# Kernel tuning notes

Measured on AMD Instinct MI355X. Metric: run time of the kernel, lower is better.

## Reference

```python
import jax, jax.numpy as jnp
import numpy as np

NUM_NODES = 1_200_000
NUM_FILLER = 200_000
NUM_PHYS = NUM_NODES - NUM_FILLER  # 1,000,000 physical nodes
NUM_MOVABLE = 900_000
NBX = NBY = 512
XL, XH, YL, YH = 0.0, 1000.0, 0.0, 1000.0
BSX = (XH - XL) / NBX
BSY = (YH - YL) / NBY
PIN_STRETCH = 1.4142135623730951
UNIT_PIN_CAP = 0.05
MAX_RATE = 1.5
MIN_RATE = 1.0 / MAX_RATE
K = 5  # max bins overlapped per dimension (span<=4.0, bin~1.95)


def _overlap_terms(lo, hi, bin_size, origin, nb):
    # lo, hi: [n] interval per node. Returns bin indices [n,K] and overlap lengths [n,K].
    il = jnp.clip(jnp.floor((lo - origin) / bin_size).astype(jnp.int32), 0, nb - 1)
    idx = il[:, None] + jnp.arange(K, dtype=jnp.int32)[None, :]
    valid = idx < nb
    idx = jnp.clip(idx, 0, nb - 1)
    b_lo = origin + idx.astype(lo.dtype) * bin_size
    ov = jnp.maximum(jnp.minimum(hi[:, None], b_lo + bin_size) - jnp.maximum(lo[:, None], b_lo), 0.0)
    return idx, jnp.where(valid, ov, 0.0)


def _forward(pos, node_size_x, node_size_y, flat_node2pin_start_map):
    P = NUM_PHYS
    sx, sy = node_size_x[:P], node_size_y[:P]
    # stretched half sizes: at least half a stretched bin
    hx = 0.5 * jnp.maximum(BSX * PIN_STRETCH, sx)
    hy = 0.5 * jnp.maximum(BSY * PIN_STRETCH, sy)
    cx = pos[:P] + 0.5 * sx
    cy = pos[NUM_NODES:NUM_NODES + P] + 0.5 * sy
    pw = (flat_node2pin_start_map[1:P + 1] - flat_node2pin_start_map[:P]).astype(pos.dtype)
    density = pw / (4.0 * hx * hy)  # pins per unit area over stretched bbox

    # stage 1: scatter stretched-bbox pin density into bin map
    ix, ovx = _overlap_terms(cx - hx, cx + hx, BSX, XL, NBX)  # [P,K]
    iy, ovy = _overlap_terms(cy - hy, cy + hy, BSY, YL, NBY)  # [P,K]
    contrib = ovx[:, :, None] * ovy[:, None, :] * density[:, None, None]  # [P,K,K]
    flat_idx = (ix[:, :, None] * NBY + iy[:, None, :]).reshape(-1)
    pin_map = jnp.zeros(NBX * NBY, dtype=pos.dtype).at[flat_idx].add(contrib.reshape(-1))

    # stage 2: pin utilization per bin, clamped adjust rate
    util = jnp.clip(pin_map / (BSX * BSY * UNIT_PIN_CAP), MIN_RATE, MAX_RATE)

    # stage 3: per movable node, integrate utilization over its (unstretched) bbox
    M = NUM_MOVABLE
    x_lo = pos[:M]
    x_hi = x_lo + node_size_x[:M]
    y_lo = pos[NUM_NODES:NUM_NODES + M]
    y_hi = y_lo + node_size_y[:M]
    jx, wx = _overlap_terms(x_lo, x_hi, BSX, XL, NBX)  # [M,K]
    jy, wy = _overlap_terms(y_lo, y_hi, BSY, YL, NBY)  # [M,K]
    u = util[jx[:, :, None] * NBY + jy[:, None, :]]  # [M,K,K]
    instance_pin_area = jnp.sum(wx[:, :, None] * wy[:, None, :] * u, axis=(1, 2))
    return instance_pin_area


def setup_inputs() -> dict:
    key = jax.random.key(0)
    k1, k2, k3, k4 = jax.random.split(key, 4)
    node_size_x = jax.random.uniform(k1, (NUM_NODES,), jnp.float32, 1.0, 4.0)
    node_size_y = jnp.full((NUM_NODES,), 2.0, jnp.float32)  # row height
    px = jax.random.uniform(k2, (NUM_NODES,), jnp.float32, 0.0, 995.0)
    py = jax.random.uniform(k3, (NUM_NODES,), jnp.float32, 0.0, 995.0)
    pos = jnp.concatenate([px, py])
    pin_counts = jax.random.randint(k4, (NUM_PHYS,), 1, 9, jnp.int32)
    flat = jnp.concatenate([jnp.zeros(1, jnp.int32), jnp.cumsum(pin_counts).astype(jnp.int32)])
    return {"pos": pos, "node_size_x": node_size_x, "node_size_y": node_size_y,
            "flat_node2pin_start_map": flat}


def reference(pos, node_size_x, node_size_y, flat_node2pin_start_map):
    return _forward(pos, node_size_x, node_size_y, flat_node2pin_start_map)
```

## Files before the change

kernel.cpp:

```cpp
#include <hip/hip_runtime.h>

#define NUM_NODES   1200000
#define NUM_FILLER  200000
#define NUM_PHYS    (NUM_NODES - NUM_FILLER)
#define NUM_MOVABLE 900000
#define NBX 512
#define NBY 512
#define NBINS (NBX * NBY)
#define BSX 1.953125f
#define BSY 1.953125f
#define PIN_STRETCH 1.4142135623730951f
#define CAP 0.19073486328125f
#define INV_CAP (1.0f / 0.19073486328125f)
#define MAX_RATE 1.5f
#define MIN_RATE (1.0f/1.5f)
#define K 5

#define TBITS   5
#define TSZ     32
#define TDIM    16
#define NTILES  (TDIM * TDIM)
#define HALO    (K - 1)
#define LTS     (TSZ + HALO)
#define NXCD    8
#define SBLK    1024
#define NPB     4096
#define NBLK    ((NUM_PHYS + NPB - 1) / NPB)
#define CAPX    1024

__device__ __forceinline__ int bin_lo(float lo) {
    int il = (int)floorf(lo / BSX);
    return min(max(il, 0), NBX - 1);
}

__device__ __forceinline__ float4 pack_rec(float cx, float cy, float hx, float hy, int pw) {
    unsigned pwm1 = (unsigned)(pw - 1) & 7u;
    unsigned ux = __float_as_uint(cx) | ((pwm1 & 1u) << 31);
    unsigned uy = __float_as_uint(cy) | (((pwm1 >> 1) & 1u) << 31);
    unsigned uz = __float_as_uint(hx) | (((pwm1 >> 2) & 1u) << 31);
    return make_float4(__uint_as_float(ux), __uint_as_float(uy),
                       __uint_as_float(uz), hy);
}

__global__ __launch_bounds__(SBLK) void sort_phys(
    const float* __restrict__ pos,
    const float* __restrict__ nsx,
    const float* __restrict__ nsy,
    const int*   __restrict__ flat,
    int*         __restrict__ cur,
    float4*      __restrict__ rec,
    float*       __restrict__ pin)
{
    __shared__ int    cnt[NTILES];
    __shared__ int    pref[NTILES];
    __shared__ int    exc[NTILES];
    __shared__ int    lofs[NTILES];
    __shared__ int    gbase[NTILES];
    __shared__ float4 stage[NPB];
    __shared__ unsigned char tileOf[NPB];

    int tid = threadIdx.x;
    int bid = blockIdx.x;
    if (tid < NTILES) cnt[tid] = 0;
    for (int i = bid * SBLK + tid; i < NBINS; i += NBLK * SBLK)
        pin[i] = 0.0f;
    __syncthreads();

    unsigned xcc;
    asm volatile("s_getreg_b32 %0, hwreg(HW_REG_XCC_ID, 0, 32)" : "=s"(xcc));
    xcc &= (NXCD - 1);

    int q = bid * SBLK + tid;
    bool valid = (4 * q + 3) < NUM_PHYS;
    float4 r4[4];
    int tl[4] = {-1, -1, -1, -1};
    if (valid) {
        const float4* pos4  = (const float4*)pos;
        const float4* posy4 = (const float4*)(pos + NUM_NODES);
        const float4* nsx4  = (const float4*)nsx;
        const float4* nsy4  = (const float4*)nsy;
        float4 px = pos4[q], py = posy4[q];
        float4 sx = nsx4[q], sy = nsy4[q];
        int4 f4 = ((const int4*)flat)[q];
        int f5 = flat[4 * q + 4];
        int pw0 = f4.y - f4.x, pw1 = f4.z - f4.y, pw2 = f4.w - f4.z, pw3 = f5 - f4.w;
        float pxs[4] = {px.x, px.y, px.z, px.w};
        float pys[4] = {py.x, py.y, py.z, py.w};
        float sxs[4] = {sx.x, sx.y, sx.z, sx.w};
        float sys[4] = {sy.x, sy.y, sy.z, sy.w};
        int   pws[4] = {pw0, pw1, pw2, pw3};
        #pragma unroll
        for (int j = 0; j < 4; ++j) {
            float hx = 0.5f * fmaxf(BSX * PIN_STRETCH, sxs[j]);
            float hy = 0.5f * fmaxf(BSY * PIN_STRETCH, sys[j]);
            float cx = pxs[j] + 0.5f * sxs[j];
            float cy = pys[j] + 0.5f * sys[j];
            r4[j] = pack_rec(cx, cy, hx, hy, pws[j]);
            int t = ((bin_lo(cx - hx) >> TBITS) << 4) | (bin_lo(cy - hy) >> TBITS);
            tl[j] = t;
            atomicAdd(&cnt[t], 1);
        }
    }
    __syncthreads();

    if (tid < NTILES) {
        int c = cnt[tid];
        gbase[tid] = (c > 0) ? atomicAdd(&cur[tid * NXCD + xcc], c) : 0;
        pref[tid] = c;
    }
    __syncthreads();
    #pragma unroll
    for (int off = 1; off < NTILES; off <<= 1) {
        int v = (tid < NTILES && tid >= off) ? pref[tid - off] : 0;
        __syncthreads();
        if (tid < NTILES) pref[tid] += v;
        __syncthreads();
    }
    if (tid < NTILES) {
        int e = pref[tid] - cnt[tid];
        exc[tid] = e;
        lofs[tid] = e;
    }
    __syncthreads();

    if (valid) {
        #pragma unroll
        for (int j = 0; j < 4; ++j) {
            int t = tl[j];
            int r = atomicAdd(&lofs[t], 1);
            stage[r] = r4[j];
            tileOf[r] = (unsigned char)t;
        }
    }
    __syncthreads();

    int total = pref[NTILES - 1];
    for (int k = tid; k < total; k += SBLK) {
        int t = tileOf[k];
        int dst = gbase[t] + (k - exc[t]);
        if (dst < CAPX)
            rec[((size_t)t * NXCD + xcc) * CAPX + dst] = stage[k];
    }
}

__global__ __launch_bounds__(1024) void accumulate_tiles(
    const float4* __restrict__ rec,
    const int*    __restrict__ cur,
    float*        __restrict__ pin)
{
    __shared__ float tileA[LTS * LTS];
    __shared__ int pref[NXCD + 1];
    int tid = threadIdx.x;
    int t = blockIdx.x;
    int bx0 = (t >> 4) * TSZ, by0 = (t & 15) * TSZ;

    for (int i = tid; i < LTS * LTS; i += 1024) tileA[i] = 0.0f;
    if (tid == 0) {
        int s = 0; pref[0] = 0;
        for (int x = 0; x < NXCD; ++x) {
            s += min(cur[t * NXCD + x], CAPX);
            pref[x + 1] = s;
        }
    }
    __syncthreads();

    int total = pref[NXCD];
    size_t tb = (size_t)t * NXCD * CAPX;
    for (int k = tid; k < total; k += 1024) {
        int x = 0;
        while (k >= pref[x + 1]) ++x;
        float4 r = rec[tb + (size_t)x * CAPX + (k - pref[x])];
        unsigned ux = __float_as_uint(r.x), uy = __float_as_uint(r.y),
                 uz = __float_as_uint(r.z);
        float pw = (float)(1 + (int)((ux >> 31) | ((uy >> 31) << 1) | ((uz >> 31) << 2)));
        float cx = __uint_as_float(ux & 0x7fffffffu);
        float cy = __uint_as_float(uy & 0x7fffffffu);
        float hx = __uint_as_float(uz & 0x7fffffffu);
        float hy = r.w;
        float d = pw / (4.0f * hx * hy);
        float lox = cx - hx, hix = cx + hx;
        float loy = cy - hy, hiy = cy + hy;
        int il = bin_lo(lox), jl = bin_lo(loy);
        int ie = min(min((int)floorf(hix / BSX), NBX - 1), il + HALO);
        int je = min(min((int)floorf(hiy / BSY), NBY - 1), jl + HALO);
        int lr = il - bx0, lc = jl - by0;
        for (int a = il; a <= ie; ++a) {
            float blo = (float)a * BSX;
            float ox = fmaxf(fminf(hix, blo + BSX) - fmaxf(lox, blo), 0.0f);
            int rowb = (lr + (a - il)) * LTS + lc;
            for (int b2 = jl; b2 <= je; ++b2) {
                float blo2 = (float)b2 * BSY;
                float oy = fmaxf(fminf(hiy, blo2 + BSY) - fmaxf(loy, blo2), 0.0f);
                float cc = ox * oy * d;
                if (cc != 0.0f) atomicAdd(&tileA[rowb + (b2 - jl)], cc);
            }
        }
    }
    __syncthreads();
    for (int i = tid; i < LTS * LTS; i += 1024) {
        float v = tileA[i];
        int r = i / LTS, c = i % LTS;
        int gx = bx0 + r, gy = by0 + c;
        if (gx >= NBX || gy >= NBY) continue;
        bool interior = (r >= HALO) && (r < TSZ) && (c >= HALO) && (c < TSZ);
        if (interior) {
            if (v != 0.0f) pin[gx * NBY + gy] = v;
        } else {
            if (v != 0.0f) atomicAdd(&pin[gx * NBY + gy], v);
        }
    }
}

__global__ __launch_bounds__(256) void gather_pin_area(
    const float* __restrict__ pos,
    const float* __restrict__ nsx,
    const float* __restrict__ nsy,
    const float* __restrict__ pin,
    float*       __restrict__ out)
{
    int q = blockIdx.x * blockDim.x + threadIdx.x;
    if (q >= NUM_MOVABLE / 4) return;

    float4 xl4 = ((const float4*)pos)[q];
    float4 yl4 = ((const float4*)(pos + NUM_NODES))[q];
    float4 sx4 = ((const float4*)nsx)[q];
    float4 sy4 = ((const float4*)nsy)[q];

    float xls[4] = {xl4.x, xl4.y, xl4.z, xl4.w};
    float yls[4] = {yl4.x, yl4.y, yl4.z, yl4.w};
    float sxs[4] = {sx4.x, sx4.y, sx4.z, sx4.w};
    float sys[4] = {sy4.x, sy4.y, sy4.z, sy4.w};
    float res[4];

    #pragma unroll
    for (int j = 0; j < 4; ++j) {
        float xlo = xls[j], xhi = xlo + sxs[j];
        float ylo = yls[j], yhi = ylo + sys[j];
        int xb = min(bin_lo(xlo), NBX - 4);
        int yb = min(bin_lo(ylo), NBY - 3);

        float u[4][3];
        #pragma unroll
        for (int a = 0; a < 4; ++a) {
            const float* __restrict__ row = pin + (xb + a) * NBY + yb;
            u[a][0] = row[0]; u[a][1] = row[1]; u[a][2] = row[2];
        }
        float wx[4], wy[3];
        #pragma unroll
        for (int kx = 0; kx < 4; ++kx) {
            float blo = (float)(xb + kx) * BSX;
            wx[kx] = fmaxf(fminf(xhi, blo + BSX) - fmaxf(xlo, blo), 0.0f);
        }
        #pragma unroll
        for (int ky = 0; ky < 3; ++ky) {
            float blo = (float)(yb + ky) * BSY;
            wy[ky] = fmaxf(fminf(yhi, blo + BSY) - fmaxf(ylo, blo), 0.0f);
        }
        float acc = 0.0f;
        #pragma unroll
        for (int a = 0; a < 4; ++a)
            #pragma unroll
            for (int b = 0; b < 3; ++b) {
                float uc = fminf(fmaxf(u[a][b] * INV_CAP, MIN_RATE), MAX_RATE);
                acc += wx[a] * wy[b] * uc;
            }
        res[j] = acc;
    }
    ((float4*)out)[q] = make_float4(res[0], res[1], res[2], res[3]);
}

__global__ __launch_bounds__(256) void scatter_pin_map_agent(
    const float* __restrict__ pos,
    const float* __restrict__ nsx,
    const float* __restrict__ nsy,
    const int*   __restrict__ flat,
    float*       __restrict__ map)
{
    int p = blockIdx.x * blockDim.x + threadIdx.x;
    if (p >= NUM_PHYS) return;
    float sx = nsx[p], sy = nsy[p];
    float hx = 0.5f * fmaxf(BSX * PIN_STRETCH, sx);
    float hy = 0.5f * fmaxf(BSY * PIN_STRETCH, sy);
    float cx = pos[p] + 0.5f * sx;
    float cy = pos[NUM_NODES + p] + 0.5f * sy;
    float pw = (float)(flat[p + 1] - flat[p]);
    float density = pw / (4.0f * hx * hy);
    float lox = cx - hx, hixv = cx + hx;
    float loy = cy - hy, hiyv = cy + hy;
    int il = bin_lo(lox), jl = bin_lo(loy);
    int ie = min(min((int)floorf(hixv / BSX), NBX - 1), il + K - 1);
    int je = min(min((int)floorf(hiyv / BSY), NBY - 1), jl + K - 1);
    for (int a = il; a <= ie; ++a) {
        float blo = (float)a * BSX;
        float ox = fmaxf(fminf(hixv, blo + BSX) - fmaxf(lox, blo), 0.0f);
        for (int b = jl; b <= je; ++b) {
            float blo2 = (float)b * BSY;
            float oy = fmaxf(fminf(hiyv, blo2 + BSY) - fmaxf(loy, blo2), 0.0f);
            float c = ox * oy * density;
            if (c != 0.0f) atomicAdd(&map[a * NBY + b], c);
        }
    }
}

__global__ __launch_bounds__(256) void gather_general(
    const float* __restrict__ pos,
    const float* __restrict__ nsx,
    const float* __restrict__ nsy,
    const float* __restrict__ pin,
    float*       __restrict__ out)
{
    int m = blockIdx.x * blockDim.x + threadIdx.x;
    if (m >= NUM_MOVABLE) return;
    float xlo = pos[m];
    float xhi = xlo + nsx[m];
    float ylo = pos[NUM_NODES + m];
    float yhi = ylo + nsy[m];
    int il = bin_lo(xlo);
    int ie = min(min((int)floorf(xhi / BSX), NBX - 1), il + K - 1);
    int jl = bin_lo(ylo);
    int je = min(min((int)floorf(yhi / BSY), NBY - 1), jl + K - 1);
    float acc = 0.0f;
    for (int a = il; a <= ie; ++a) {
        float blo = (float)a * BSX;
        float wxv = fmaxf(fminf(xhi, blo + BSX) - fmaxf(xlo, blo), 0.0f);
        const float* __restrict__ row = pin + a * NBY;
        for (int b2 = jl; b2 <= je; ++b2) {
            float blo2 = (float)b2 * BSY;
            float wyv = fmaxf(fminf(yhi, blo2 + BSY) - fmaxf(ylo, blo2), 0.0f);
            float uc = fminf(fmaxf(row[b2] * INV_CAP, MIN_RATE), MAX_RATE);
            acc += wxv * wyv * uc;
        }
    }
    out[m] = acc;
}

extern "C" void kernel_launch(void* const* d_in, const int* in_sizes, int n_in,
                              void* d_out, int out_size, void* d_ws, size_t ws_size,
                              hipStream_t stream) {
    const float* pos  = (const float*)d_in[0];
    const float* nsx  = (const float*)d_in[1];
    const float* nsy  = (const float*)d_in[2];
    const int*   flat = (const int*)d_in[3];
    float* out = (float*)d_out;

    const size_t NSLOT = (size_t)NTILES * NXCD * CAPX;
    char* wsb = (char*)d_ws;
    float*  pin = (float*)wsb;
    int*    cur = (int*)(wsb + (size_t)NBINS * 4);
    float4* rec = (float4*)(wsb + (size_t)NBINS * 4 + 32768);
    size_t needed = (size_t)NBINS * 4 + 32768 + NSLOT * 16;

    dim3 blk(256);
    if (ws_size >= needed) {
        hipMemsetAsync(cur, 0, (size_t)NTILES * NXCD * sizeof(int), stream);
        sort_phys<<<NBLK, dim3(SBLK), 0, stream>>>(pos, nsx, nsy, flat, cur, rec, pin);
        accumulate_tiles<<<NTILES, dim3(1024), 0, stream>>>(rec, cur, pin);
        gather_pin_area<<<(NUM_MOVABLE / 4 + 255) / 256, blk, 0, stream>>>(pos, nsx, nsy, pin, out);
    } else {
        hipMemsetAsync(pin, 0, (size_t)NBINS * 4, stream);
        scatter_pin_map_agent<<<(NUM_PHYS + 255) / 256, blk, 0, stream>>>(pos, nsx, nsy, flat, pin);
        gather_general<<<(NUM_MOVABLE + 255) / 256, blk, 0, stream>>>(pos, nsx, nsy, pin, out);
    }
}
```

Measured before the change: 140.2 us.

## Replace global atomic tile bucketing with per-block sorted segments and offset tables

The sort kernel no longer reserves space in per-tile, per-XCD buckets with global atomics. Each block writes its locally tile-sorted records contiguously to its own segment and publishes per-tile counts and offsets. The accumulate kernel then builds a prefix over the source blocks and binary-searches it to locate each record. This removes the memset, the global atomics and the CAPX overflow truncation, at the cost of a per-record binary search and loads that are less contiguous within each tile.

After: 138.6 us. No clear change (-1.1%).

```diff
diff --git a/kernel.cpp b/kernel.cpp
--- a/kernel.cpp
+++ b/kernel.cpp
@@ -22,11 +22,10 @@
 #define NTILES  (TDIM * TDIM)
 #define HALO    (K - 1)
 #define LTS     (TSZ + HALO)
-#define NXCD    8
 #define SBLK    1024
 #define NPB     4096
 #define NBLK    ((NUM_PHYS + NPB - 1) / NPB)
-#define CAPX    1024
+#define MSTR    256
 
 __device__ __forceinline__ int bin_lo(float lo) {
     int il = (int)floorf(lo / BSX);
@@ -47,7 +46,8 @@
     const float* __restrict__ nsx,
     const float* __restrict__ nsy,
     const int*   __restrict__ flat,
-    int*         __restrict__ cur,
+    int*         __restrict__ cntArr,
+    int*         __restrict__ offArr,
     float4*      __restrict__ rec,
     float*       __restrict__ pin)
 {
@@ -55,20 +55,13 @@
     __shared__ int    pref[NTILES];
     __shared__ int    exc[NTILES];
     __shared__ int    lofs[NTILES];
-    __shared__ int    gbase[NTILES];
     __shared__ float4 stage[NPB];
-    __shared__ unsigned char tileOf[NPB];
-
     int tid = threadIdx.x;
     int bid = blockIdx.x;
     if (tid < NTILES) cnt[tid] = 0;
     for (int i = bid * SBLK + tid; i < NBINS; i += NBLK * SBLK)
         pin[i] = 0.0f;
     __syncthreads();
-
-    unsigned xcc;
-    asm volatile("s_getreg_b32 %0, hwreg(HW_REG_XCC_ID, 0, 32)" : "=s"(xcc));
-    xcc &= (NXCD - 1);
 
     int q = bid * SBLK + tid;
     bool valid = (4 * q + 3) < NUM_PHYS;
@@ -83,12 +76,11 @@
         float4 sx = nsx4[q], sy = nsy4[q];
         int4 f4 = ((const int4*)flat)[q];
         int f5 = flat[4 * q + 4];
-        int pw0 = f4.y - f4.x, pw1 = f4.z - f4.y, pw2 = f4.w - f4.z, pw3 = f5 - f4.w;
         float pxs[4] = {px.x, px.y, px.z, px.w};
         float pys[4] = {py.x, py.y, py.z, py.w};
         float sxs[4] = {sx.x, sx.y, sx.z, sx.w};
         float sys[4] = {sy.x, sy.y, sy.z, sy.w};
-        int   pws[4] = {pw0, pw1, pw2, pw3};
+        int   pws[4] = {f4.y - f4.x, f4.z - f4.y, f4.w - f4.z, f5 - f4.w};
         #pragma unroll
         for (int j = 0; j < 4; ++j) {
             float hx = 0.5f * fmaxf(BSX * PIN_STRETCH, sxs[j]);
@@ -103,11 +95,7 @@
     }
     __syncthreads();
 
-    if (tid < NTILES) {
-        int c = cnt[tid];
-        gbase[tid] = (c > 0) ? atomicAdd(&cur[tid * NXCD + xcc], c) : 0;
-        pref[tid] = c;
-    }
+    if (tid < NTILES) pref[tid] = cnt[tid];
     __syncthreads();
     #pragma unroll
     for (int off = 1; off < NTILES; off <<= 1) {
@@ -120,56 +108,61 @@
         int e = pref[tid] - cnt[tid];
         exc[tid] = e;
         lofs[tid] = e;
+        cntArr[tid * MSTR + bid] = cnt[tid];
+        offArr[tid * MSTR + bid] = e;
     }
     __syncthreads();
 
     if (valid) {
         #pragma unroll
         for (int j = 0; j < 4; ++j) {
-            int t = tl[j];
-            int r = atomicAdd(&lofs[t], 1);
+            int r = atomicAdd(&lofs[tl[j]], 1);
             stage[r] = r4[j];
-            tileOf[r] = (unsigned char)t;
         }
     }
     __syncthreads();
 
     int total = pref[NTILES - 1];
-    for (int k = tid; k < total; k += SBLK) {
-        int t = tileOf[k];
-        int dst = gbase[t] + (k - exc[t]);
-        if (dst < CAPX)
-            rec[((size_t)t * NXCD + xcc) * CAPX + dst] = stage[k];
-    }
+    float4* __restrict__ dst = rec + (size_t)bid * NPB;
+    for (int k = tid; k < total; k += SBLK)
+        dst[k] = stage[k];
 }
 
 __global__ __launch_bounds__(1024) void accumulate_tiles(
     const float4* __restrict__ rec,
-    const int*    __restrict__ cur,
+    const int*    __restrict__ cntArr,
+    const int*    __restrict__ offArr,
     float*        __restrict__ pin)
 {
     __shared__ float tileA[LTS * LTS];
-    __shared__ int pref[NXCD + 1];
+    __shared__ int cntB[NBLK];
+    __shared__ int offB[NBLK];
+    __shared__ int prefB[NBLK + 1];
     int tid = threadIdx.x;
     int t = blockIdx.x;
     int bx0 = (t >> 4) * TSZ, by0 = (t & 15) * TSZ;
 
     for (int i = tid; i < LTS * LTS; i += 1024) tileA[i] = 0.0f;
+    if (tid < NBLK) {
+        cntB[tid] = cntArr[t * MSTR + tid];
+        offB[tid] = offArr[t * MSTR + tid];
+    }
+    __syncthreads();
     if (tid == 0) {
-        int s = 0; pref[0] = 0;
-        for (int x = 0; x < NXCD; ++x) {
-            s += min(cur[t * NXCD + x], CAPX);
-            pref[x + 1] = s;
-        }
-    }
-    __syncthreads();
-
-    int total = pref[NXCD];
-    size_t tb = (size_t)t * NXCD * CAPX;
+        int s = 0;
+        for (int b = 0; b < NBLK; ++b) { prefB[b] = s; s += cntB[b]; }
+        prefB[NBLK] = s;
+    }
+    __syncthreads();
+
+    int total = prefB[NBLK];
     for (int k = tid; k < total; k += 1024) {
-        int x = 0;
-        while (k >= pref[x + 1]) ++x;
-        float4 r = rec[tb + (size_t)x * CAPX + (k - pref[x])];
+        int lo = 0, hi = NBLK;
+        while (hi - lo > 1) {
+            int mid = (lo + hi) >> 1;
+            if (k >= prefB[mid]) lo = mid; else hi = mid;
+        }
+        float4 r = rec[(size_t)lo * NPB + offB[lo] + (k - prefB[lo])];
         unsigned ux = __float_as_uint(r.x), uy = __float_as_uint(r.y),
                  uz = __float_as_uint(r.z);
         float pw = (float)(1 + (int)((ux >> 31) | ((uy >> 31) << 1) | ((uz >> 31) << 2)));
@@ -343,18 +336,20 @@
     const int*   flat = (const int*)d_in[3];
     float* out = (float*)d_out;
 
-    const size_t NSLOT = (size_t)NTILES * NXCD * CAPX;
     char* wsb = (char*)d_ws;
-    float*  pin = (float*)wsb;
-    int*    cur = (int*)(wsb + (size_t)NBINS * 4);
-    float4* rec = (float4*)(wsb + (size_t)NBINS * 4 + 32768);
-    size_t needed = (size_t)NBINS * 4 + 32768 + NSLOT * 16;
+    float*  pin    = (float*)wsb;
+    int*    cntArr = (int*)(wsb + (size_t)NBINS * 4);
+    int*    offArr = cntArr + (size_t)NTILES * MSTR;
+    float4* rec    = (float4*)(wsb + (size_t)NBINS * 4
+                               + 2 * (size_t)NTILES * MSTR * 4);
+    size_t needed = (size_t)NBINS * 4 + 2 * (size_t)NTILES * MSTR * 4
+                  + (size_t)NBLK * NPB * 16;
 
     dim3 blk(256);
     if (ws_size >= needed) {
-        hipMemsetAsync(cur, 0, (size_t)NTILES * NXCD * sizeof(int), stream);
-        sort_phys<<<NBLK, dim3(SBLK), 0, stream>>>(pos, nsx, nsy, flat, cur, rec, pin);
-        accumulate_tiles<<<NTILES, dim3(1024), 0, stream>>>(rec, cur, pin);
+        sort_phys<<<NBLK, dim3(SBLK), 0, stream>>>(pos, nsx, nsy, flat,
+                                                   cntArr, offArr, rec, pin);
+        accumulate_tiles<<<NTILES, dim3(1024), 0, stream>>>(rec, cntArr, offArr, pin);
         gather_pin_area<<<(NUM_MOVABLE / 4 + 255) / 256, blk, 0, stream>>>(pos, nsx, nsy, pin, out);
     } else {
         hipMemsetAsync(pin, 0, (size_t)NBINS * 4, stream);
```
